# Optimization experiments

Measured on AMD Instinct MI355X. Metric: run time of the kernel, lower is better.

The kernel has to match this reference:

```python
import jax, jax.numpy as jnp
import numpy as np

CHUNK = 4096
DECAY = 0.99
EPS = 1e-5


def setup_inputs() -> dict:
    key = jax.random.key(0)
    k1, k2, k3, k4 = jax.random.split(key, 4)
    z = jax.random.normal(k1, (32, 64, 32, 32), dtype=jnp.float32)
    codebook = jax.random.normal(k2, (8192, 64), dtype=jnp.float32)
    cluster_size = jax.random.uniform(k3, (8192,), dtype=jnp.float32)
    embed_avg = jax.random.normal(k4, (8192, 64), dtype=jnp.float32)
    return {"z": z, "codebook": codebook, "cluster_size": cluster_size, "embed_avg": embed_avg}


def _nearest_indices(vectors, codebook):
    """Chunked fp32 squared-L2 nearest-neighbor search (matches _nearest_indices)."""
    cb = codebook.astype(jnp.float32)
    c2 = jnp.sum(cb * cb, axis=1)  # [K]

    def chunk_fn(chunk):
        v = chunk.astype(jnp.float32)  # [CHUNK, D]
        d = jnp.sum(v * v, axis=1, keepdims=True) + c2[None, :] - 2.0 * (v @ cb.T)
        return jnp.argmin(d, axis=1)

    n, d = vectors.shape  # n divisible by CHUNK by construction
    chunks = vectors.reshape(n // CHUNK, CHUNK, d)
    return jax.lax.map(chunk_fn, chunks).reshape(-1)


def reference(z, codebook, cluster_size, embed_avg):
    B, C, H, W = z.shape
    K = codebook.shape[0]
    # [B,C,H,W] -> [N,C]
    vectors = jnp.transpose(z, (0, 2, 3, 1)).reshape(-1, C)
    N = vectors.shape[0]

    indices = _nearest_indices(vectors, codebook)  # [N] int
    quantized = jnp.transpose(codebook[indices].reshape(B, H, W, C), (0, 3, 1, 2))

    # commitment loss (codebook learned via EMA, so only encoder side differentiable)
    vq_loss = jnp.mean((jax.lax.stop_gradient(quantized) - z) ** 2)
    # straight-through estimator
    quantized_st = z + jax.lax.stop_gradient(quantized - z)

    # code usage statistics
    counts = jax.ops.segment_sum(jnp.ones((N,), jnp.float32), indices, num_segments=K)
    avg_probs = counts / N
    perplexity = jnp.exp(-jnp.sum(avg_probs * jnp.log(avg_probs + 1e-10)))
    active_codes = jnp.sum(counts > 0).astype(jnp.int32)

    # EMA update (scatter-add accumulation + Laplace-smoothed normalization)
    sums = jax.ops.segment_sum(vectors.astype(jnp.float32), indices, num_segments=K)
    new_cluster_size = DECAY * cluster_size + (1.0 - DECAY) * counts
    new_embed_avg = DECAY * embed_avg + (1.0 - DECAY) * sums
    n_total = jnp.sum(new_cluster_size)
    smoothed = (new_cluster_size + EPS) / (n_total + K * EPS) * n_total
    new_codebook = new_embed_avg / smoothed[:, None]

    return (quantized_st, indices, vq_loss, perplexity, active_codes,
            new_codebook, new_cluster_size, new_embed_avg)
```

## Files before the change

kernel.cpp:

```cpp
#include <hip/hip_runtime.h>
#include <math.h>

typedef unsigned short u16;
typedef unsigned int u32;
typedef unsigned long long u64;
typedef __attribute__((ext_vector_type(8))) short short8;
typedef __attribute__((ext_vector_type(4))) float f32x4;

#define NVEC   32768
#define DIMV   64
#define KC     8192
#define NKCH   8
#define CHK    1024
#define HW     1024
#define BPLANE 65536
#define NSTEP  (CHK / 32)

#define OFF_Q    0
#define OFF_IDX  2097152
#define OFF_LOSS 2129920
#define OFF_PPL  2129921
#define OFF_ACT  2129922
#define OFF_NCB  2129923
#define OFF_NCS  2654211
#define OFF_NEA  2662403

#define WS_COUNTS 0
#define WS_SCAL   8192
#define WS_C2     8200
#define WS_MINP   16400
#define WS_OFFS   81936
#define WS_PERM   90128
#define WS_CBF    122896

__device__ __forceinline__ u16 f2bf(float x) {
    u32 u = __float_as_uint(x);
    u += 0x7fffu + ((u >> 16) & 1u);
    return (u16)(u >> 16);
}
__device__ __forceinline__ float bf2f(u16 h) {
    return __uint_as_float(((u32)h) << 16);
}
__device__ __forceinline__ u32 fmono(float f) {
    u32 b = __float_as_uint(f);
    return (b & 0x80000000u) ? ~b : (b | 0x80000000u);
}

__global__ __launch_bounds__(256) void cbsplit_kernel(const float* __restrict__ cb,
                                                      u16* __restrict__ cbf,
                                                      float* __restrict__ c2,
                                                      float* __restrict__ counts,
                                                      float* __restrict__ scal,
                                                      u64* __restrict__ minp) {
    const int t = threadIdx.x;
    const int gid = blockIdx.x * 256 + t;
    if (gid < 8192) counts[gid] = 0.f;
    if (gid < 8) scal[gid] = 0.f;
    if (gid < NVEC) minp[gid] = ~0ull;

    const int k = blockIdx.x * 4 + (t >> 6);
    const int d = t & 63;
    const int idx = k * DIMV + d;
    float x = cb[idx];
    u16 hb = f2bf(x);  float fh = bf2f(hb);
    float r1 = x - fh; u16 mb = f2bf(r1); float fm = bf2f(mb);
    float r2 = r1 - fm; u16 lb = f2bf(r2);
    const int ti = k >> 4, row = k & 15;
    const int half = d >> 5;
    const int cg = (d >> 3) & 3;
    const int le = row + cg * 16;
    u16* base = cbf + (size_t)ti * 3072 + le * 8 + (d & 7);
    base[(0 + half) * 512] = hb;
    base[(2 + half) * 512] = mb;
    base[(4 + half) * 512] = lb;
    float s = x * x;
    for (int off = 32; off > 0; off >>= 1) s += __shfl_down(s, off, 64);
    if (d == 0) c2[k] = s;
}

#define NN_COMPUTE(Bh0, Bh1, Bm0, Bm1, Bl0, Bl1, CM, NTI)                          \
    _Pragma("unroll")                                                               \
    for (int i = 0; i < 2; ++i) {                                                   \
        f32x4 acc = {CM, CM, CM, CM};                                               \
        acc = __builtin_amdgcn_mfma_f32_16x16x32_bf16(A[i][0][0], Bh0, acc, 0, 0, 0);\
        acc = __builtin_amdgcn_mfma_f32_16x16x32_bf16(A[i][0][1], Bh1, acc, 0, 0, 0);\
        acc = __builtin_amdgcn_mfma_f32_16x16x32_bf16(A[i][1][0], Bh0, acc, 0, 0, 0);\
        acc = __builtin_amdgcn_mfma_f32_16x16x32_bf16(A[i][1][1], Bh1, acc, 0, 0, 0);\
        acc = __builtin_amdgcn_mfma_f32_16x16x32_bf16(A[i][0][0], Bm0, acc, 0, 0, 0);\
        acc = __builtin_amdgcn_mfma_f32_16x16x32_bf16(A[i][0][1], Bm1, acc, 0, 0, 0);\
        acc = __builtin_amdgcn_mfma_f32_16x16x32_bf16(A[i][1][0], Bm0, acc, 0, 0, 0);\
        acc = __builtin_amdgcn_mfma_f32_16x16x32_bf16(A[i][1][1], Bm1, acc, 0, 0, 0);\
        acc = __builtin_amdgcn_mfma_f32_16x16x32_bf16(A[i][2][0], Bh0, acc, 0, 0, 0);\
        acc = __builtin_amdgcn_mfma_f32_16x16x32_bf16(A[i][2][1], Bh1, acc, 0, 0, 0);\
        acc = __builtin_amdgcn_mfma_f32_16x16x32_bf16(A[i][0][0], Bl0, acc, 0, 0, 0);\
        acc = __builtin_amdgcn_mfma_f32_16x16x32_bf16(A[i][0][1], Bl1, acc, 0, 0, 0);\
        _Pragma("unroll")                                                           \
        for (int r = 0; r < 4; ++r) {                                               \
            float a = acc[r];                                                       \
            if (a > bestv[i][r]) { bestv[i][r] = a; bestn[i][r] = (NTI); }          \
        }                                                                           \
    }

#define STAGE(B, ST)                                                                \
    _Pragma("unroll")                                                               \
    for (int j = 0; j < 3; ++j) {                                                   \
        const u16* gs = pcbf + (size_t)(ST) * 6144 + j * 2048 + tl * 8;             \
        u16* ld = &ldsb[B][j * 2048 + wv * 512];                                    \
        __builtin_amdgcn_global_load_lds(                                           \
            (const __attribute__((address_space(1))) void*)gs,                      \
            (__attribute__((address_space(3))) void*)ld, 16, 0, 0);                 \
    }

__global__ __launch_bounds__(256, 4) void nn_kernel(const float* __restrict__ z,
                                                    const u16* __restrict__ cbf,
                                                    const float* __restrict__ c2,
                                                    u64* __restrict__ minp) {
    __shared__ __align__(16) u16 ldsb[2][6144];
    const int tl = threadIdx.x;
    const int l  = tl & 63;
    const int wv = tl >> 6;
    const int vg = blockIdx.x;
    const int kc = blockIdx.y;
    const int m0 = vg * 128 + wv * 32;
    const int lr = l & 15;
    const int lg = l >> 4;

    short8 A[2][3][2];
#pragma unroll
    for (int i = 0; i < 2; ++i) {
        const int vec = m0 + i * 16 + lr;
        const float* zp = z + (size_t)(vec >> 10) * BPLANE + (vec & 1023);
#pragma unroll
        for (int s = 0; s < 2; ++s) {
            short8 ah, am, al;
#pragma unroll
            for (int e = 0; e < 8; ++e) {
                const int k = s * 32 + lg * 8 + e;
                float x = zp[k * HW];
                u16 hb = f2bf(x);   float fh = bf2f(hb);
                float r1 = x - fh;  u16 mb = f2bf(r1); float fm = bf2f(mb);
                float r2 = r1 - fm; u16 lb = f2bf(r2);
                ah[e] = (short)hb; am[e] = (short)mb; al[e] = (short)lb;
            }
            A[i][0][s] = ah; A[i][1][s] = am; A[i][2][s] = al;
        }
    }

    float bestv[2][4];
    int   bestn[2][4];
#pragma unroll
    for (int i = 0; i < 2; ++i)
#pragma unroll
        for (int r = 0; r < 4; ++r) { bestv[i][r] = -3.4e38f; bestn[i][r] = 0; }

    const int code_base = kc * CHK;
    const float* pc2 = c2 + code_base + lr;
    const u16* pcbf = cbf + (size_t)kc * (CHK / 16) * 3072;

    STAGE(0, 0)
    __syncthreads();

    for (int st = 0; st < NSTEP; ++st) {
        const int b = st & 1;
        const float cmA = -0.5f * pc2[(st * 2) * 16];
        const float cmB = -0.5f * pc2[(st * 2 + 1) * 16];
        if (st + 1 < NSTEP) { STAGE(b ^ 1, st + 1) }

        const u16* baseA = &ldsb[b][l * 8];
        {
            short8 h0 = *(const short8*)(baseA);
            short8 h1 = *(const short8*)(baseA + 512);
            short8 m0f = *(const short8*)(baseA + 1024);
            short8 m1f = *(const short8*)(baseA + 1536);
            short8 l0f = *(const short8*)(baseA + 2048);
            short8 l1f = *(const short8*)(baseA + 2560);
            NN_COMPUTE(h0, h1, m0f, m1f, l0f, l1f, cmA, st * 2)
        }
        {
            const u16* baseB = baseA + 3072;
            short8 h0 = *(const short8*)(baseB);
            short8 h1 = *(const short8*)(baseB + 512);
            short8 m0f = *(const short8*)(baseB + 1024);
            short8 m1f = *(const short8*)(baseB + 1536);
            short8 l0f = *(const short8*)(baseB + 2048);
            short8 l1f = *(const short8*)(baseB + 2560);
            NN_COMPUTE(h0, h1, m0f, m1f, l0f, l1f, cmB, st * 2 + 1)
        }
        __syncthreads();
    }

#pragma unroll
    for (int i = 0; i < 2; ++i)
#pragma unroll
        for (int r = 0; r < 4; ++r) {
            float v = bestv[i][r];
            int idx = bestn[i][r] * 16 + lr;
#pragma unroll
            for (int mk = 1; mk < 16; mk <<= 1) {
                float ov = __shfl_xor(v, mk, 64);
                int   oi = __shfl_xor(idx, mk, 64);
                if (ov > v || (ov == v && oi < idx)) { v = ov; idx = oi; }
            }
            if (lr == 0) {
                const int vec = m0 + i * 16 + lg * 4 + r;
                const u64 pack = ((u64)fmono(-v) << 32) | (u32)(code_base + idx);
                atomicMin(&minp[vec], pack);
            }
        }
}

__global__ __launch_bounds__(256) void gather_kernel(const float* __restrict__ z,
                                                     const float* __restrict__ cb,
                                                     const u64* __restrict__ minp,
                                                     float* __restrict__ out,
                                                     float* __restrict__ counts,
                                                     float* __restrict__ scal) {
    const int n = blockIdx.x * 256 + threadIdx.x;
    const int cg = blockIdx.y;
    const int bi = (int)(u32)(minp[n] & 0xFFFFFFFFu);
    if (cg == 0) {
        out[OFF_IDX + n] = (float)bi;
        atomicAdd(&counts[bi], 1.0f);
    }

    const int b = n >> 10, h = n & 1023;
    const size_t off = (size_t)b * BPLANE + (size_t)cg * 16 * HW + h;
    const float* zp = z + off;
    const float* cp = cb + (size_t)bi * DIMV + cg * 16;
    float* qp = out + OFF_Q + off;
    float acc = 0.f;
#pragma unroll
    for (int c = 0; c < 16; ++c) {
        float zv = zp[c * HW];
        float q = cp[c];
        float df = q - zv;
        acc = fmaf(df, df, acc);
        qp[c * HW] = zv + df;
    }
    for (int off2 = 32; off2 > 0; off2 >>= 1) acc += __shfl_down(acc, off2, 64);
    __shared__ float red[4];
    if ((threadIdx.x & 63) == 0) red[threadIdx.x >> 6] = acc;
    __syncthreads();
    if (threadIdx.x == 0) atomicAdd(&scal[0], (red[0] + red[1]) + (red[2] + red[3]));
}

__global__ __launch_bounds__(256) void prefix_kernel(const float* __restrict__ counts,
                                                     const float* __restrict__ cs,
                                                     float* __restrict__ out,
                                                     int* __restrict__ offs,
                                                     float* __restrict__ scal) {
    __shared__ int part[256];
    __shared__ float r0[4], r1[4], r2[4];
    const int t = threadIdx.x;
    const int base = t * 32;
    int loc[32];
    int s = 0;
    float sncs = 0.f, spl = 0.f, sact = 0.f;
#pragma unroll
    for (int j = 0; j < 32; ++j) {
        const int c = (int)counts[base + j];
        loc[j] = s; s += c;
        const float cnt = (float)c;
        const float ncs = 0.99f * cs[base + j] + 0.01f * cnt;
        out[OFF_NCS + base + j] = ncs;
        const float p = cnt * (1.0f / 32768.0f);
        spl += p * logf(p + 1e-10f);
        sact += (cnt > 0) ? 1.f : 0.f;
        sncs += ncs;
    }
    part[t] = s;
    __syncthreads();
    for (int off = 1; off < 256; off <<= 1) {
        int v = (t >= off) ? part[t - off] : 0;
        __syncthreads();
        part[t] += v;
        __syncthreads();
    }
    const int excl = part[t] - s;
#pragma unroll
    for (int j = 0; j < 32; ++j) offs[base + j] = excl + loc[j];

    for (int off = 32; off > 0; off >>= 1) {
        sncs += __shfl_down(sncs, off, 64);
        spl  += __shfl_down(spl,  off, 64);
        sact += __shfl_down(sact, off, 64);
    }
    const int w = t >> 6;
    if ((t & 63) == 0) { r0[w] = sncs; r1[w] = spl; r2[w] = sact; }
    __syncthreads();
    if (t == 0) {
        const float nt = (r0[0] + r0[1]) + (r0[2] + r0[3]);
        scal[1] = nt;
        out[OFF_LOSS] = scal[0] * (1.0f / 2097152.0f);
        out[OFF_PPL]  = expf(-((r1[0] + r1[1]) + (r1[2] + r1[3])));
        out[OFF_ACT]  = (r2[0] + r2[1]) + (r2[2] + r2[3]);
    }
}

__global__ __launch_bounds__(256) void scatter_kernel(const float* __restrict__ outIdx,
                                                      int* __restrict__ offs,
                                                      int* __restrict__ perm) {
    const int n = blockIdx.x * 256 + threadIdx.x;
    const int bi = (int)outIdx[n];
    const int pos = atomicAdd(&offs[bi], 1);
    perm[pos] = n;
}

__global__ __launch_bounds__(256) void segsum_kernel(const float* __restrict__ z,
                                                     const float* __restrict__ counts,
                                                     const int* __restrict__ offs,
                                                     const int* __restrict__ perm,
                                                     const float* __restrict__ ea,
                                                     float* __restrict__ out,
                                                     const float* __restrict__ scal) {
    const int w = threadIdx.x >> 6;
    const int c = threadIdx.x & 63;
    const int k = blockIdx.x * 4 + w;
    const int end = offs[k];
    const int cnt = (int)counts[k];
    float s = 0.f;
    for (int m = end - cnt; m < end; ++m) {
        const int n = perm[m];
        s += z[(size_t)(n >> 10) * BPLANE + (size_t)c * HW + (n & 1023)];
    }
    const int idx = k * DIMV + c;
    const float nea = 0.99f * ea[idx] + 0.01f * s;
    out[OFF_NEA + idx] = nea;
    const float nt = scal[1];
    const float ncs = out[OFF_NCS + k];
    const float sm = ((ncs + 1e-5f) / (nt + 0.08192f)) * nt;
    out[OFF_NCB + idx] = nea / sm;
}

extern "C" void kernel_launch(void* const* d_in, const int* in_sizes, int n_in,
                              void* d_out, int out_size, void* d_ws, size_t ws_size,
                              hipStream_t stream) {
    const float* z  = (const float*)d_in[0];
    const float* cb = (const float*)d_in[1];
    const float* cs = (const float*)d_in[2];
    const float* ea = (const float*)d_in[3];
    float* out = (float*)d_out;
    float* ws  = (float*)d_ws;

    float* counts = ws + WS_COUNTS;
    float* scal   = ws + WS_SCAL;
    float* c2     = ws + WS_C2;
    u64*   minp   = (u64*)(ws + WS_MINP);
    int*   offs   = (int*)(ws + WS_OFFS);
    int*   perm   = (int*)(ws + WS_PERM);
    u16*   cbf    = (u16*)(ws + WS_CBF);

    cbsplit_kernel<<<KC / 4, 256, 0, stream>>>(cb, cbf, c2, counts, scal, minp);
    nn_kernel<<<dim3(256, NKCH), 256, 0, stream>>>(z, cbf, c2, minp);
    gather_kernel<<<dim3(NVEC / 256, 4), 256, 0, stream>>>(z, cb, minp, out, counts, scal);
    prefix_kernel<<<1, 256, 0, stream>>>(counts, cs, out, offs, scal);
    scatter_kernel<<<NVEC / 256, 256, 0, stream>>>(out + OFF_IDX, offs, perm);
    segsum_kernel<<<KC / 4, 256, 0, stream>>>(z, counts, offs, perm, ea, out, scal);
}
```

Before: 253.1 us.

## Switch nearest-neighbour search to 32x32x16 MFMA with codes-as-rows layout

Rewrites the distance GEMM to use 32x32x16 bf16 MFMA, with codebook tiles as the A operand and z vectors as B, so each lane accumulates one vector across 32 codes. The codebook prep layout is changed to 32-code tiles to match. The argmin reduction becomes a per-lane running best plus a single cross-half shuffle instead of a 16-lane butterfly. The c2 bias is now added after the MFMA chain instead of seeding the accumulator. Occupancy hint drops from 4 to 3 blocks per SM to allow more registers.

```diff
diff --git a/kernel.cpp b/kernel.cpp
--- a/kernel.cpp
+++ b/kernel.cpp
@@ -5,7 +5,7 @@
 typedef unsigned int u32;
 typedef unsigned long long u64;
 typedef __attribute__((ext_vector_type(8))) short short8;
-typedef __attribute__((ext_vector_type(4))) float f32x4;
+typedef __attribute__((ext_vector_type(16))) float f32x16;
 
 #define NVEC   32768
 #define DIMV   64
@@ -65,41 +65,18 @@
     u16 hb = f2bf(x);  float fh = bf2f(hb);
     float r1 = x - fh; u16 mb = f2bf(r1); float fm = bf2f(mb);
     float r2 = r1 - fm; u16 lb = f2bf(r2);
-    const int ti = k >> 4, row = k & 15;
-    const int half = d >> 5;
-    const int cg = (d >> 3) & 3;
-    const int le = row + cg * 16;
-    u16* base = cbf + (size_t)ti * 3072 + le * 8 + (d & 7);
-    base[(0 + half) * 512] = hb;
-    base[(2 + half) * 512] = mb;
-    base[(4 + half) * 512] = lb;
+    const int ti = k >> 5, c5 = k & 31;
+    const int ks = d >> 4;
+    const int g = (d >> 3) & 1;
+    const int e = d & 7;
+    u16* base = cbf + (size_t)ti * 6144 + ks * 512 + (c5 + 32 * g) * 8 + e;
+    base[0 * 2048] = hb;
+    base[1 * 2048] = mb;
+    base[2 * 2048] = lb;
     float s = x * x;
     for (int off = 32; off > 0; off >>= 1) s += __shfl_down(s, off, 64);
     if (d == 0) c2[k] = s;
 }
-
-#define NN_COMPUTE(Bh0, Bh1, Bm0, Bm1, Bl0, Bl1, CM, NTI)                          \
-    _Pragma("unroll")                                                               \
-    for (int i = 0; i < 2; ++i) {                                                   \
-        f32x4 acc = {CM, CM, CM, CM};                                               \
-        acc = __builtin_amdgcn_mfma_f32_16x16x32_bf16(A[i][0][0], Bh0, acc, 0, 0, 0);\
-        acc = __builtin_amdgcn_mfma_f32_16x16x32_bf16(A[i][0][1], Bh1, acc, 0, 0, 0);\
-        acc = __builtin_amdgcn_mfma_f32_16x16x32_bf16(A[i][1][0], Bh0, acc, 0, 0, 0);\
-        acc = __builtin_amdgcn_mfma_f32_16x16x32_bf16(A[i][1][1], Bh1, acc, 0, 0, 0);\
-        acc = __builtin_amdgcn_mfma_f32_16x16x32_bf16(A[i][0][0], Bm0, acc, 0, 0, 0);\
-        acc = __builtin_amdgcn_mfma_f32_16x16x32_bf16(A[i][0][1], Bm1, acc, 0, 0, 0);\
-        acc = __builtin_amdgcn_mfma_f32_16x16x32_bf16(A[i][1][0], Bm0, acc, 0, 0, 0);\
-        acc = __builtin_amdgcn_mfma_f32_16x16x32_bf16(A[i][1][1], Bm1, acc, 0, 0, 0);\
-        acc = __builtin_amdgcn_mfma_f32_16x16x32_bf16(A[i][2][0], Bh0, acc, 0, 0, 0);\
-        acc = __builtin_amdgcn_mfma_f32_16x16x32_bf16(A[i][2][1], Bh1, acc, 0, 0, 0);\
-        acc = __builtin_amdgcn_mfma_f32_16x16x32_bf16(A[i][0][0], Bl0, acc, 0, 0, 0);\
-        acc = __builtin_amdgcn_mfma_f32_16x16x32_bf16(A[i][0][1], Bl1, acc, 0, 0, 0);\
-        _Pragma("unroll")                                                           \
-        for (int r = 0; r < 4; ++r) {                                               \
-            float a = acc[r];                                                       \
-            if (a > bestv[i][r]) { bestv[i][r] = a; bestn[i][r] = (NTI); }          \
-        }                                                                           \
-    }
 
 #define STAGE(B, ST)                                                                \
     _Pragma("unroll")                                                               \
@@ -111,7 +88,7 @@
             (__attribute__((address_space(3))) void*)ld, 16, 0, 0);                 \
     }
 
-__global__ __launch_bounds__(256, 4) void nn_kernel(const float* __restrict__ z,
+__global__ __launch_bounds__(256, 3) void nn_kernel(const float* __restrict__ z,
                                                     const u16* __restrict__ cbf,
                                                     const float* __restrict__ c2,
                                                     u64* __restrict__ minp) {
@@ -122,91 +99,78 @@
     const int vg = blockIdx.x;
     const int kc = blockIdx.y;
     const int m0 = vg * 128 + wv * 32;
-    const int lr = l & 15;
-    const int lg = l >> 4;
-
-    short8 A[2][3][2];
-#pragma unroll
-    for (int i = 0; i < 2; ++i) {
-        const int vec = m0 + i * 16 + lr;
+    const int hi = l >> 5;
+    const int vec = m0 + (l & 31);
+
+    short8 Z[3][4];
+    {
         const float* zp = z + (size_t)(vec >> 10) * BPLANE + (vec & 1023);
 #pragma unroll
-        for (int s = 0; s < 2; ++s) {
-            short8 ah, am, al;
+        for (int ks = 0; ks < 4; ++ks) {
+            short8 zh, zm, zl;
 #pragma unroll
             for (int e = 0; e < 8; ++e) {
-                const int k = s * 32 + lg * 8 + e;
+                const int k = ks * 16 + hi * 8 + e;
                 float x = zp[k * HW];
                 u16 hb = f2bf(x);   float fh = bf2f(hb);
                 float r1 = x - fh;  u16 mb = f2bf(r1); float fm = bf2f(mb);
                 float r2 = r1 - fm; u16 lb = f2bf(r2);
-                ah[e] = (short)hb; am[e] = (short)mb; al[e] = (short)lb;
+                zh[e] = (short)hb; zm[e] = (short)mb; zl[e] = (short)lb;
             }
-            A[i][0][s] = ah; A[i][1][s] = am; A[i][2][s] = al;
+            Z[0][ks] = zh; Z[1][ks] = zm; Z[2][ks] = zl;
         }
     }
 
-    float bestv[2][4];
-    int   bestn[2][4];
-#pragma unroll
-    for (int i = 0; i < 2; ++i)
-#pragma unroll
-        for (int r = 0; r < 4; ++r) { bestv[i][r] = -3.4e38f; bestn[i][r] = 0; }
+    float bestv = -3.4e38f;
+    int   besti = 0;
 
     const int code_base = kc * CHK;
-    const float* pc2 = c2 + code_base + lr;
-    const u16* pcbf = cbf + (size_t)kc * (CHK / 16) * 3072;
+    const float* pc2 = c2 + code_base;
+    const u16* pcbf = cbf + (size_t)kc * (CHK / 32) * 6144;
 
     STAGE(0, 0)
     __syncthreads();
 
     for (int st = 0; st < NSTEP; ++st) {
         const int b = st & 1;
-        const float cmA = -0.5f * pc2[(st * 2) * 16];
-        const float cmB = -0.5f * pc2[(st * 2 + 1) * 16];
         if (st + 1 < NSTEP) { STAGE(b ^ 1, st + 1) }
 
-        const u16* baseA = &ldsb[b][l * 8];
-        {
-            short8 h0 = *(const short8*)(baseA);
-            short8 h1 = *(const short8*)(baseA + 512);
-            short8 m0f = *(const short8*)(baseA + 1024);
-            short8 m1f = *(const short8*)(baseA + 1536);
-            short8 l0f = *(const short8*)(baseA + 2048);
-            short8 l1f = *(const short8*)(baseA + 2560);
-            NN_COMPUTE(h0, h1, m0f, m1f, l0f, l1f, cmA, st * 2)
+        const u16* base0 = &ldsb[b][l * 8];
+        f32x16 acc = {0.f, 0.f, 0.f, 0.f, 0.f, 0.f, 0.f, 0.f,
+                      0.f, 0.f, 0.f, 0.f, 0.f, 0.f, 0.f, 0.f};
+#pragma unroll
+        for (int ks = 0; ks < 4; ++ks) {
+            short8 ch = *(const short8*)(base0 + 0 * 2048 + ks * 512);
+            short8 cm = *(const short8*)(base0 + 1 * 2048 + ks * 512);
+            short8 cl = *(const short8*)(base0 + 2 * 2048 + ks * 512);
+            acc = __builtin_amdgcn_mfma_f32_32x32x16_bf16(ch, Z[0][ks], acc, 0, 0, 0);
+            acc = __builtin_amdgcn_mfma_f32_32x32x16_bf16(ch, Z[1][ks], acc, 0, 0, 0);
+            acc = __builtin_amdgcn_mfma_f32_32x32x16_bf16(cm, Z[0][ks], acc, 0, 0, 0);
+            acc = __builtin_amdgcn_mfma_f32_32x32x16_bf16(cm, Z[1][ks], acc, 0, 0, 0);
+            acc = __builtin_amdgcn_mfma_f32_32x32x16_bf16(cl, Z[0][ks], acc, 0, 0, 0);
+            acc = __builtin_amdgcn_mfma_f32_32x32x16_bf16(ch, Z[2][ks], acc, 0, 0, 0);
         }
-        {
-            const u16* baseB = baseA + 3072;
-            short8 h0 = *(const short8*)(baseB);
-            short8 h1 = *(const short8*)(baseB + 512);
-            short8 m0f = *(const short8*)(baseB + 1024);
-            short8 m1f = *(const short8*)(baseB + 1536);
-            short8 l0f = *(const short8*)(baseB + 2048);
-            short8 l1f = *(const short8*)(baseB + 2560);
-            NN_COMPUTE(h0, h1, m0f, m1f, l0f, l1f, cmB, st * 2 + 1)
+
+        const float* c2s = pc2 + st * 32 + hi * 4;
+#pragma unroll
+        for (int r = 0; r < 16; ++r) {
+            const int rc = (r & 3) + 8 * (r >> 2);
+            const float val = fmaf(-0.5f, c2s[rc], acc[r]);
+            const int ci = st * 32 + rc + hi * 4;
+            if (val > bestv) { bestv = val; besti = ci; }
         }
         __syncthreads();
     }
 
-#pragma unroll
-    for (int i = 0; i < 2; ++i)
-#pragma unroll
-        for (int r = 0; r < 4; ++r) {
-            float v = bestv[i][r];
-            int idx = bestn[i][r] * 16 + lr;
-#pragma unroll
-            for (int mk = 1; mk < 16; mk <<= 1) {
-                float ov = __shfl_xor(v, mk, 64);
-                int   oi = __shfl_xor(idx, mk, 64);
-                if (ov > v || (ov == v && oi < idx)) { v = ov; idx = oi; }
-            }
-            if (lr == 0) {
-                const int vec = m0 + i * 16 + lg * 4 + r;
-                const u64 pack = ((u64)fmono(-v) << 32) | (u32)(code_base + idx);
-                atomicMin(&minp[vec], pack);
-            }
-        }
+    {
+        const float ov = __shfl_xor(bestv, 32, 64);
+        const int   oi = __shfl_xor(besti, 32, 64);
+        if (ov > bestv || (ov == bestv && oi < besti)) { bestv = ov; besti = oi; }
+    }
+    if (l < 32) {
+        const u64 pack = ((u64)fmono(-bestv) << 32) | (u32)(code_base + besti);
+        atomicMin(&minp[m0 + l], pack);
+    }
 }
 
 __global__ __launch_bounds__(256) void gather_kernel(const float* __restrict__ z,
```

Result: slower. 277.6 us (+9.7%).
